# Optimization experiments

Measured on AMD Instinct MI355X. Metric: run time of the kernel, lower is better.

## Reference

```python
import jax, jax.numpy as jnp
import numpy as np

B, S, D = 4, 1024, 1024
DH = D // 8  # q/k projection dim


def setup_inputs() -> dict:
    key = jax.random.key(0)
    ks = jax.random.split(key, 16)
    std = 0.02
    inp = {
        "drums": jax.random.normal(ks[0], (B, S, D), jnp.float32),
        "vocals": jax.random.normal(ks[1], (B, S, D), jnp.float32),
        "bass": jax.random.normal(ks[2], (B, S, D), jnp.float32),
        "other": jax.random.normal(ks[3], (B, S, D), jnp.float32),
        # Linear weights stored [in, out] (transposed vs torch's [out, in])
        "DqW": jax.random.normal(ks[4], (D, DH), jnp.float32) * std,
        "Dqb": jax.random.normal(ks[5], (DH,), jnp.float32) * std,
        "DkW": jax.random.normal(ks[6], (D, DH), jnp.float32) * std,
        "Dkb": jax.random.normal(ks[7], (DH,), jnp.float32) * std,
        "DvW": jax.random.normal(ks[8], (D, D), jnp.float32) * std,
        "Dvb": jax.random.normal(ks[9], (D,), jnp.float32) * std,
        "VqW": jax.random.normal(ks[10], (D, DH), jnp.float32) * std,
        "Vqb": jax.random.normal(ks[11], (DH,), jnp.float32) * std,
        "VkW": jax.random.normal(ks[12], (D, DH), jnp.float32) * std,
        "Vkb": jax.random.normal(ks[13], (DH,), jnp.float32) * std,
        "VvW": jax.random.normal(ks[14], (D, D), jnp.float32) * std,
        "Vvb": jax.random.normal(ks[15], (D,), jnp.float32) * std,
    }
    return inp


def reference(drums, vocals, bass, other,
              DqW, Dqb, DkW, Dkb, DvW, Dvb,
              VqW, Vqb, VkW, Vkb, VvW, Vvb):
    d_model = drums.shape[-1]
    lin = lambda x, W, b: jnp.einsum("bsd,de->bse", x, W) + b
    # drums uses D_* projections; vocals/bass/other all use V_* (faithful to source)
    q = jnp.concatenate([lin(drums, DqW, Dqb), lin(vocals, VqW, Vqb),
                         lin(bass, VqW, Vqb), lin(other, VqW, Vqb)], axis=-2)
    k = jnp.concatenate([lin(drums, DkW, Dkb), lin(vocals, VkW, Vkb),
                         lin(bass, VkW, Vkb), lin(other, VkW, Vkb)], axis=-2)
    v = jnp.concatenate([lin(drums, DvW, Dvb), lin(vocals, VvW, Vvb),
                         lin(bass, VvW, Vvb), lin(other, VvW, Vvb)], axis=-2)
    # scores: [B, 4S, 4S]; dropout is identity at inference
    scores = jnp.einsum("bqe,bke->bqk", q, k) / jnp.sqrt(jnp.asarray(d_model, q.dtype))
    attn = jax.nn.softmax(scores, axis=-1)
    out = jnp.einsum("bqk,bkd->bqd", attn, v)  # [B, 4S, D]
    return out.mean(axis=-2)  # [B, D]
```

## Files before the change

### kernel.cpp

```cpp
#include <hip/hip_runtime.h>
#include <hip/hip_bf16.h>

typedef __bf16 bf16x8 __attribute__((ext_vector_type(8)));
typedef float  f32x4  __attribute__((ext_vector_type(4)));

#define MFMA(a, b, c) __builtin_amdgcn_mfma_f32_16x16x32_bf16((a), (b), (c), 0, 0, 0)

static constexpr float SC_L2E = 0.03125f * 1.44269504088896341f;
static constexpr float INV_NQ = 1.0f / 4096.0f;

__device__ inline bf16x8 ld_cvt_bf8(const float* __restrict__ p) {
    f32x4 x0 = *(const f32x4*)p;
    f32x4 x1 = *(const f32x4*)(p + 4);
    bf16x8 r;
    r[0] = (__bf16)x0[0]; r[1] = (__bf16)x0[1]; r[2] = (__bf16)x0[2]; r[3] = (__bf16)x0[3];
    r[4] = (__bf16)x1[0]; r[5] = (__bf16)x1[1]; r[6] = (__bf16)x1[2]; r[7] = (__bf16)x1[3];
    return r;
}

__global__ __launch_bounds__(256) void kT(const float* __restrict__ Dq, const float* __restrict__ Vq,
                                          const float* __restrict__ Dk, const float* __restrict__ Vk,
                                          __bf16* __restrict__ Wt) {
    __shared__ float tile[64][65];
    int bx = blockIdx.x;
    int m = bx >> 5, rt = (bx >> 1) & 15, ct = bx & 1;
    const float* W = (m == 0) ? Dq : (m == 1) ? Vq : (m == 2) ? Dk : Vk;
    int t = threadIdx.x;
    int tr = t >> 6, tc = t & 63;
#pragma unroll
    for (int i = 0; i < 16; i++) {
        int rl = tr + i * 4;
        tile[rl][tc] = W[(size_t)(rt * 64 + rl) * 128 + ct * 64 + tc];
    }
    __syncthreads();
#pragma unroll
    for (int i = 0; i < 16; i++) {
        int cl = tr + i * 4;
        Wt[(size_t)m * 131072 + (size_t)(ct * 64 + cl) * 1024 + rt * 64 + tc] = (__bf16)tile[tc][cl];
    }
}

__global__ __launch_bounds__(256) void kProj(
    const float* __restrict__ drums, const float* __restrict__ vocals,
    const float* __restrict__ bass,  const float* __restrict__ other,
    const float* __restrict__ Dqb, const float* __restrict__ Vqb,
    const float* __restrict__ Dkb, const float* __restrict__ Vkb,
    const __bf16* __restrict__ Wt, __bf16* __restrict__ Qb, __bf16* __restrict__ Kb) {
    int grow0 = blockIdx.x * 16;
    int b    = grow0 >> 12;
    int r4   = grow0 & 4095;
    int stem = r4 >> 10;
    int rin  = r4 & 1023;

    const float* X = (stem == 0) ? drums : (stem == 1) ? vocals : (stem == 2) ? bass : other;
    const __bf16* WQ = Wt + (size_t)((stem == 0) ? 0 : 1) * 131072;
    const __bf16* WK = Wt + (size_t)((stem == 0) ? 2 : 3) * 131072;
    const float* bQ = (stem == 0) ? Dqb : Vqb;
    const float* bK = (stem == 0) ? Dkb : Vkb;

    int lane = threadIdx.x & 63, wid = threadIdx.x >> 6;
    int l16 = lane & 15, g = lane >> 4;

    f32x4 aQ[2], aK[2];
#pragma unroll
    for (int j = 0; j < 2; j++) { aQ[j] = (f32x4){0.f,0.f,0.f,0.f}; aK[j] = (f32x4){0.f,0.f,0.f,0.f}; }

    const float*  xr  = X  + ((size_t)b * 1024 + rin + l16) * 1024;
    const __bf16* wq0 = WQ + (size_t)(wid * 32 + l16) * 1024;
    const __bf16* wq1 = wq0 + 16 * 1024;
    const __bf16* wk0 = WK + (size_t)(wid * 32 + l16) * 1024;
    const __bf16* wk1 = wk0 + 16 * 1024;

    for (int k0 = 0; k0 < 1024; k0 += 32) {
        int ko = k0 + g * 8;
        bf16x8 a = ld_cvt_bf8(xr + ko);
        aQ[0] = MFMA(a, *(const bf16x8*)(wq0 + ko), aQ[0]);
        aQ[1] = MFMA(a, *(const bf16x8*)(wq1 + ko), aQ[1]);
        aK[0] = MFMA(a, *(const bf16x8*)(wk0 + ko), aK[0]);
        aK[1] = MFMA(a, *(const bf16x8*)(wk1 + ko), aK[1]);
    }
    size_t obase = (size_t)b * 4096 + (size_t)stem * 1024 + rin;
#pragma unroll
    for (int cf = 0; cf < 2; cf++) {
        int col = (wid * 2 + cf) * 16 + l16;
        float bvq = bQ[col], bvk = bK[col];
#pragma unroll
        for (int r = 0; r < 4; r++) {
            int row = g * 4 + r;
            Qb[(obase + row) * 128 + col] = (__bf16)(aQ[cf][r] + bvq);
            Kb[(obase + row) * 128 + col] = (__bf16)(aK[cf][r] + bvk);
        }
    }
}

__global__ __launch_bounds__(256) void kRowSum(const __bf16* __restrict__ Qb,
                                               const __bf16* __restrict__ Kb,
                                               float* __restrict__ lsum) {
    __shared__ uint4 ktile[1024];
    int bx = blockIdx.x;
    int cc = bx & 7, tile = (bx >> 3) & 31, b = bx >> 8;
    int lane = threadIdx.x & 63, wid = threadIdx.x >> 6;
    int l16 = lane & 15, g = lane >> 4;
    int R  = tile * 128 + wid * 32;
    int C0 = cc * 512;
    const __bf16* Qr = Qb + (size_t)b * 4096 * 128;
    const __bf16* Kr = Kb + (size_t)b * 4096 * 128;

    bf16x8 a[2][4];
#pragma unroll
    for (int rf = 0; rf < 2; rf++)
#pragma unroll
        for (int kf = 0; kf < 4; kf++)
            a[rf][kf] = *(const bf16x8*)(Qr + (size_t)(R + rf * 16 + l16) * 128 + kf * 32 + g * 8);

    int sr = threadIdx.x >> 2, sseg = threadIdx.x & 3;
    char* kbc = (char*)ktile;
    int swm = (sr & 7) << 4;

    uint4 st[4];
    {
        const char* src = (const char*)(Kr + (size_t)(C0 + sr) * 128) + sseg * 64;
#pragma unroll
        for (int j = 0; j < 4; j++) st[j] = *(const uint4*)(src + j * 16);
    }

    float rs[2][4] = {};
    for (int s = 0; s < 8; ++s) {
        __syncthreads();
#pragma unroll
        for (int j = 0; j < 4; j++)
            *(uint4*)(kbc + sr * 256 + ((sseg * 64 + j * 16) ^ swm)) = st[j];
        __syncthreads();
        if (s < 7) {
            const char* src = (const char*)(Kr + (size_t)(C0 + (s + 1) * 64 + sr) * 128) + sseg * 64;
#pragma unroll
            for (int j = 0; j < 4; j++) st[j] = *(const uint4*)(src + j * 16);
        }
#pragma unroll
        for (int ctl = 0; ctl < 4; ++ctl) {
            int r2 = ctl * 16 + l16;
            int rm = (r2 & 7) << 4;
            f32x4 acc0 = (f32x4){0.f,0.f,0.f,0.f};
            f32x4 acc1 = (f32x4){0.f,0.f,0.f,0.f};
#pragma unroll
            for (int kf = 0; kf < 4; kf++) {
                bf16x8 bv = *(const bf16x8*)(kbc + r2 * 256 + ((kf * 64 + g * 16) ^ rm));
                acc0 = MFMA(a[0][kf], bv, acc0);
                acc1 = MFMA(a[1][kf], bv, acc1);
            }
#pragma unroll
            for (int r = 0; r < 4; r++) {
                rs[0][r] += exp2f(acc0[r] * SC_L2E);
                rs[1][r] += exp2f(acc1[r] * SC_L2E);
            }
        }
    }
#pragma unroll
    for (int rf = 0; rf < 2; rf++)
#pragma unroll
        for (int r = 0; r < 4; r++) {
            float v = rs[rf][r];
#pragma unroll
            for (int m = 1; m < 16; m <<= 1) v += __shfl_xor(v, m);
            if (l16 == 0) atomicAdd(&lsum[(size_t)b * 4096 + R + rf * 16 + g * 4 + r], v);
        }
}

__global__ __launch_bounds__(256) void kInv(const float* __restrict__ lsum, float* __restrict__ linv) {
    int i = (blockIdx.x * 256 + threadIdx.x) * 4;
    f32x4 v = *(const f32x4*)(lsum + i);
    f32x4 r = (f32x4){1.f / v[0], 1.f / v[1], 1.f / v[2], 1.f / v[3]};
    *(f32x4*)(linv + i) = r;
}

__global__ __launch_bounds__(256) void kColSum(const __bf16* __restrict__ Qb,
                                               const __bf16* __restrict__ Kb,
                                               const float* __restrict__ linv,
                                               float* __restrict__ wsum) {
    __shared__ uint4 qtile[1024];
    __shared__ float li[512];
    int bx = blockIdx.x;
    int rc = bx & 7, tile = (bx >> 3) & 31, b = bx >> 8;
    int lane = threadIdx.x & 63, wid = threadIdx.x >> 6;
    int l16 = lane & 15, g = lane >> 4;
    int C  = tile * 128 + wid * 32;
    int R0 = rc * 512;
    const __bf16* Qr = Qb + (size_t)b * 4096 * 128;
    const __bf16* Kr = Kb + (size_t)b * 4096 * 128;

    if (threadIdx.x < 128)
        *(f32x4*)(li + threadIdx.x * 4) = *(const f32x4*)(linv + (size_t)b * 4096 + R0 + threadIdx.x * 4);

    bf16x8 kb[2][4];
#pragma unroll
    for (int cf = 0; cf < 2; cf++)
#pragma unroll
        for (int kf = 0; kf < 4; kf++)
            kb[cf][kf] = *(const bf16x8*)(Kr + (size_t)(C + cf * 16 + l16) * 128 + kf * 32 + g * 8);

    int sr = threadIdx.x >> 2, sseg = threadIdx.x & 3;
    char* qbc = (char*)qtile;
    int swm = (sr & 7) << 4;

    uint4 st[4];
    {
        const char* src = (const char*)(Qr + (size_t)(R0 + sr) * 128) + sseg * 64;
#pragma unroll
        for (int j = 0; j < 4; j++) st[j] = *(const uint4*)(src + j * 16);
    }

    float cs[2] = {0.f, 0.f};
    for (int s = 0; s < 8; ++s) {
        __syncthreads();
#pragma unroll
        for (int j = 0; j < 4; j++)
            *(uint4*)(qbc + sr * 256 + ((sseg * 64 + j * 16) ^ swm)) = st[j];
        __syncthreads();
        if (s < 7) {
            const char* src = (const char*)(Qr + (size_t)(R0 + (s + 1) * 64 + sr) * 128) + sseg * 64;
#pragma unroll
            for (int j = 0; j < 4; j++) st[j] = *(const uint4*)(src + j * 16);
        }
#pragma unroll
        for (int ctl = 0; ctl < 4; ++ctl) {
            int r2 = ctl * 16 + l16;
            int rm = (r2 & 7) << 4;
            f32x4 acc0 = (f32x4){0.f,0.f,0.f,0.f};
            f32x4 acc1 = (f32x4){0.f,0.f,0.f,0.f};
#pragma unroll
            for (int kf = 0; kf < 4; kf++) {
                bf16x8 av = *(const bf16x8*)(qbc + r2 * 256 + ((kf * 64 + g * 16) ^ rm));
                acc0 = MFMA(av, kb[0][kf], acc0);
                acc1 = MFMA(av, kb[1][kf], acc1);
            }
            int ib = s * 64 + ctl * 16 + g * 4;
#pragma unroll
            for (int r = 0; r < 4; r++) {
                float lv = li[ib + r];
                cs[0] += exp2f(acc0[r] * SC_L2E) * lv;
                cs[1] += exp2f(acc1[r] * SC_L2E) * lv;
            }
        }
    }
#pragma unroll
    for (int cf = 0; cf < 2; cf++) {
        float v = cs[cf];
        v += __shfl_xor(v, 16);
        v += __shfl_xor(v, 32);
        if (lane < 16) atomicAdd(&wsum[(size_t)b * 4096 + C + cf * 16 + lane], v);
    }
}

__global__ __launch_bounds__(256) void kY(
    const float* __restrict__ drums, const float* __restrict__ vocals,
    const float* __restrict__ bass,  const float* __restrict__ other,
    const float* __restrict__ wsum, float* __restrict__ y, float* __restrict__ alpha) {
    __shared__ float ws[16];
    int bx = blockIdx.x;
    int b = bx >> 8, stem = (bx >> 6) & 3, kc = bx & 63;
    const float* X = (stem == 0) ? drums : (stem == 1) ? vocals : (stem == 2) ? bass : other;
    int t = threadIdx.x;
    float wv = 0.f;
    if (t < 16) { wv = wsum[(size_t)b * 4096 + stem * 1024 + kc * 16 + t] * INV_NQ; ws[t] = wv; }
    __syncthreads();

    f32x4 acc = (f32x4){0.f, 0.f, 0.f, 0.f};
    const float* xp = X + ((size_t)b * 1024 + kc * 16) * 1024 + t * 4;
#pragma unroll 4
    for (int i = 0; i < 16; i++) {
        f32x4 xv = *(const f32x4*)(xp + (size_t)i * 1024);
        float wvi = ws[i];
        acc[0] += wvi * xv[0]; acc[1] += wvi * xv[1]; acc[2] += wvi * xv[2]; acc[3] += wvi * xv[3];
    }
    int seg = (stem == 0) ? 0 : 1;
    float* yp = y + ((size_t)b * 2 + seg) * 1024 + t * 4;
    atomicAdd(yp + 0, acc[0]); atomicAdd(yp + 1, acc[1]);
    atomicAdd(yp + 2, acc[2]); atomicAdd(yp + 3, acc[3]);

    if (t < 16) {
        float s = wv;
        s += __shfl_xor(s, 1); s += __shfl_xor(s, 2);
        s += __shfl_xor(s, 4); s += __shfl_xor(s, 8);
        if (t == 0) atomicAdd(alpha + b * 2 + seg, s);
    }
}

__global__ __launch_bounds__(256) void kFinal(
    const float* __restrict__ DvW, const float* __restrict__ Dvb,
    const float* __restrict__ VvW, const float* __restrict__ Vvb,
    const float* __restrict__ y, const float* __restrict__ alpha,
    float* __restrict__ out) {
    __shared__ float yD[32], yV[32];
    int bx = blockIdx.x;
    int b = bx >> 7, dstripe = (bx >> 5) & 3, kc = bx & 31;
    int t = threadIdx.x;
    if (t < 32) {
        yD[t] = y[((size_t)b * 2 + 0) * 1024 + kc * 32 + t];
        yV[t] = y[((size_t)b * 2 + 1) * 1024 + kc * 32 + t];
    }
    __syncthreads();

    int d = dstripe * 256 + t;
    const float* pD = DvW + (size_t)(kc * 32) * 1024 + d;
    const float* pV = VvW + (size_t)(kc * 32) * 1024 + d;
    float acc = 0.f;
#pragma unroll 4
    for (int k = 0; k < 32; k++)
        acc += yD[k] * pD[(size_t)k * 1024] + yV[k] * pV[(size_t)k * 1024];
    if (kc == 0) acc += alpha[b * 2] * Dvb[d] + alpha[b * 2 + 1] * Vvb[d];
    atomicAdd(out + (size_t)b * 1024 + d, acc);
}

extern "C" void kernel_launch(void* const* d_in, const int* in_sizes, int n_in,
                              void* d_out, int out_size, void* d_ws, size_t ws_size,
                              hipStream_t stream) {
    const float* drums  = (const float*)d_in[0];
    const float* vocals = (const float*)d_in[1];
    const float* bass   = (const float*)d_in[2];
    const float* other  = (const float*)d_in[3];
    const float* DqW = (const float*)d_in[4];
    const float* Dqb = (const float*)d_in[5];
    const float* DkW = (const float*)d_in[6];
    const float* Dkb = (const float*)d_in[7];
    const float* DvW = (const float*)d_in[8];
    const float* Dvb = (const float*)d_in[9];
    const float* VqW = (const float*)d_in[10];
    const float* Vqb = (const float*)d_in[11];
    const float* VkW = (const float*)d_in[12];
    const float* Vkb = (const float*)d_in[13];
    const float* VvW = (const float*)d_in[14];
    const float* Vvb = (const float*)d_in[15];
    float* out = (float*)d_out;

    char* ws = (char*)d_ws;
    __bf16* Qb   = (__bf16*)(ws);
    __bf16* Kb   = (__bf16*)(ws + (4u << 20));
    __bf16* Wt   = (__bf16*)(ws + (8u << 20));
    float*  lsum = (float*)(ws + (9u << 20));
    float*  wsum = (float*)(ws + (9u << 20) + (64u << 10));
    float*  y    = (float*)(ws + (9u << 20) + (128u << 10));
    float*  alph = (float*)(ws + (9u << 20) + (160u << 10));
    float*  linv = (float*)(ws + (9u << 20) + (192u << 10));

    hipMemsetAsync(lsum, 0, (160u << 10) + 32, stream);
    hipMemsetAsync(out, 0, (size_t)out_size * sizeof(float), stream);

    kT<<<128, 256, 0, stream>>>(DqW, VqW, DkW, VkW, Wt);
    kProj<<<1024, 256, 0, stream>>>(drums, vocals, bass, other, Dqb, Vqb, Dkb, Vkb, Wt, Qb, Kb);
    kRowSum<<<1024, 256, 0, stream>>>(Qb, Kb, lsum);
    kInv<<<16, 256, 0, stream>>>(lsum, linv);
    kColSum<<<1024, 256, 0, stream>>>(Qb, Kb, linv, wsum);
    kY<<<1024, 256, 0, stream>>>(drums, vocals, bass, other, wsum, y, alph);
    kFinal<<<512, 256, 0, stream>>>(DvW, Dvb, VvW, Vvb, y, alph, out);
}
```

Before: 355.5 us.

## Split-K Q/K projection with LDS-staged swizzled X tiles and atomic accumulation

```diff
diff --git a/kernel.cpp b/kernel.cpp
--- a/kernel.cpp
+++ b/kernel.cpp
@@ -18,6 +18,13 @@
     return r;
 }
 
+__device__ inline bf16x8 cvt2_bf8(f32x4 a, f32x4 b) {
+    bf16x8 r;
+    r[0] = (__bf16)a[0]; r[1] = (__bf16)a[1]; r[2] = (__bf16)a[2]; r[3] = (__bf16)a[3];
+    r[4] = (__bf16)b[0]; r[5] = (__bf16)b[1]; r[6] = (__bf16)b[2]; r[7] = (__bf16)b[3];
+    return r;
+}
+
 __global__ __launch_bounds__(256) void kT(const float* __restrict__ Dq, const float* __restrict__ Vq,
                                           const float* __restrict__ Dk, const float* __restrict__ Vk,
                                           __bf16* __restrict__ Wt) {
@@ -40,57 +47,107 @@
     }
 }
 
-__global__ __launch_bounds__(256) void kProj(
+__global__ __launch_bounds__(256) void kProjP(
     const float* __restrict__ drums, const float* __restrict__ vocals,
     const float* __restrict__ bass,  const float* __restrict__ other,
-    const float* __restrict__ Dqb, const float* __restrict__ Vqb,
-    const float* __restrict__ Dkb, const float* __restrict__ Vkb,
-    const __bf16* __restrict__ Wt, __bf16* __restrict__ Qb, __bf16* __restrict__ Kb) {
-    int grow0 = blockIdx.x * 16;
-    int b    = grow0 >> 12;
-    int r4   = grow0 & 4095;
-    int stem = r4 >> 10;
-    int rin  = r4 & 1023;
+    const __bf16* __restrict__ Wt, float* __restrict__ Qf, float* __restrict__ Kf) {
+    __shared__ char xt[8192];
+    int bx = blockIdx.x;
+    int kc = bx & 3, rt = (bx >> 2) & 15, bs = bx >> 6;
+    int b = bs >> 2, stem = bs & 3;
+    int rin = rt * 64;
+    int k0b = kc * 256;
 
     const float* X = (stem == 0) ? drums : (stem == 1) ? vocals : (stem == 2) ? bass : other;
     const __bf16* WQ = Wt + (size_t)((stem == 0) ? 0 : 1) * 131072;
     const __bf16* WK = Wt + (size_t)((stem == 0) ? 2 : 3) * 131072;
-    const float* bQ = (stem == 0) ? Dqb : Vqb;
-    const float* bK = (stem == 0) ? Dkb : Vkb;
-
-    int lane = threadIdx.x & 63, wid = threadIdx.x >> 6;
+
+    int t = threadIdx.x;
+    int lane = t & 63, wid = t >> 6;
     int l16 = lane & 15, g = lane >> 4;
 
-    f32x4 aQ[2], aK[2];
-#pragma unroll
-    for (int j = 0; j < 2; j++) { aQ[j] = (f32x4){0.f,0.f,0.f,0.f}; aK[j] = (f32x4){0.f,0.f,0.f,0.f}; }
-
-    const float*  xr  = X  + ((size_t)b * 1024 + rin + l16) * 1024;
-    const __bf16* wq0 = WQ + (size_t)(wid * 32 + l16) * 1024;
-    const __bf16* wq1 = wq0 + 16 * 1024;
-    const __bf16* wk0 = WK + (size_t)(wid * 32 + l16) * 1024;
-    const __bf16* wk1 = wk0 + 16 * 1024;
-
-    for (int k0 = 0; k0 < 1024; k0 += 32) {
-        int ko = k0 + g * 8;
-        bf16x8 a = ld_cvt_bf8(xr + ko);
-        aQ[0] = MFMA(a, *(const bf16x8*)(wq0 + ko), aQ[0]);
-        aQ[1] = MFMA(a, *(const bf16x8*)(wq1 + ko), aQ[1]);
-        aK[0] = MFMA(a, *(const bf16x8*)(wk0 + ko), aK[0]);
-        aK[1] = MFMA(a, *(const bf16x8*)(wk1 + ko), aK[1]);
-    }
-    size_t obase = (size_t)b * 4096 + (size_t)stem * 1024 + rin;
-#pragma unroll
-    for (int cf = 0; cf < 2; cf++) {
-        int col = (wid * 2 + cf) * 16 + l16;
-        float bvq = bQ[col], bvk = bK[col];
-#pragma unroll
-        for (int r = 0; r < 4; r++) {
-            int row = g * 4 + r;
-            Qb[(obase + row) * 128 + col] = (__bf16)(aQ[cf][r] + bvq);
-            Kb[(obase + row) * 128 + col] = (__bf16)(aK[cf][r] + bvk);
-        }
-    }
+    const __bf16* Wm = (wid < 2) ? WQ : WK;
+    int colbase = (wid & 1) * 64;
+    float* Pf = (wid < 2) ? Qf : Kf;
+
+    int srow = t >> 2, sseg = t & 3;
+    const float* xsrc = X + ((size_t)b * 1024 + rin + srow) * 1024 + k0b + sseg * 16;
+    int swz = (srow & 7) << 4;
+    char* wrp = xt + srow * 128;
+
+    f32x4 st[4];
+#define LOADST(s) { const float* p_ = xsrc + (s) * 64; \
+    st[0] = *(const f32x4*)p_; st[1] = *(const f32x4*)(p_ + 4); \
+    st[2] = *(const f32x4*)(p_ + 8); st[3] = *(const f32x4*)(p_ + 12); }
+    LOADST(0);
+
+    f32x4 acc[4][4];
+#pragma unroll
+    for (int i = 0; i < 4; i++)
+#pragma unroll
+        for (int j = 0; j < 4; j++) acc[i][j] = (f32x4){0.f, 0.f, 0.f, 0.f};
+
+    for (int s = 0; s < 4; ++s) {
+        if (s) __syncthreads();
+        bf16x8 c0 = cvt2_bf8(st[0], st[1]);
+        bf16x8 c1 = cvt2_bf8(st[2], st[3]);
+        *(uint4*)(wrp + ((sseg * 32) ^ swz))      = *(uint4*)&c0;
+        *(uint4*)(wrp + ((sseg * 32 + 16) ^ swz)) = *(uint4*)&c1;
+        __syncthreads();
+        if (s < 3) LOADST(s + 1);
+#pragma unroll
+        for (int kk = 0; kk < 64; kk += 32) {
+            bf16x8 bfr[4];
+#pragma unroll
+            for (int cf = 0; cf < 4; cf++)
+                bfr[cf] = *(const bf16x8*)(Wm + (size_t)(colbase + cf * 16 + l16) * 1024
+                                           + k0b + s * 64 + kk + g * 8);
+#pragma unroll
+            for (int rf = 0; rf < 4; rf++) {
+                int row = rf * 16 + l16;
+                bf16x8 av = *(const bf16x8*)(xt + row * 128
+                                             + (((kk + g * 8) * 2) ^ ((row & 7) << 4)));
+#pragma unroll
+                for (int cf = 0; cf < 4; cf++)
+                    acc[rf][cf] = MFMA(av, bfr[cf], acc[rf][cf]);
+            }
+        }
+    }
+#undef LOADST
+
+    size_t grow = (size_t)b * 4096 + (size_t)stem * 1024 + rin;
+#pragma unroll
+    for (int rf = 0; rf < 4; rf++)
+#pragma unroll
+        for (int cf = 0; cf < 4; cf++) {
+            int col = colbase + cf * 16 + l16;
+#pragma unroll
+            for (int i = 0; i < 4; i++)
+                atomicAdd(&Pf[(grow + rf * 16 + g * 4 + i) * 128 + col], acc[rf][cf][i]);
+        }
+}
+
+__global__ __launch_bounds__(256) void kBias(
+    const float* __restrict__ Qf, const float* __restrict__ Kf,
+    const float* __restrict__ Dqb, const float* __restrict__ Vqb,
+    const float* __restrict__ Dkb, const float* __restrict__ Vkb,
+    __bf16* __restrict__ Qb, __bf16* __restrict__ Kb) {
+    int gid = blockIdx.x * 256 + threadIdx.x;
+    int qk  = gid >> 18;
+    int rem = gid & 262143;
+    int row = rem >> 4, ch = rem & 15;
+    int stem = (row >> 10) & 3;
+    const float* Pf   = qk ? Kf : Qf;
+    const float* bias = qk ? ((stem == 0) ? Dkb : Vkb) : ((stem == 0) ? Dqb : Vqb);
+    __bf16* Out = qk ? Kb : Qb;
+    int col = ch * 8;
+    f32x4 v0 = *(const f32x4*)(Pf + (size_t)row * 128 + col);
+    f32x4 v1 = *(const f32x4*)(Pf + (size_t)row * 128 + col + 4);
+    f32x4 b0 = *(const f32x4*)(bias + col);
+    f32x4 b1 = *(const f32x4*)(bias + col + 4);
+    bf16x8 r = cvt2_bf8((f32x4){v0[0]+b0[0], v0[1]+b0[1], v0[2]+b0[2], v0[3]+b0[3]},
+                        (f32x4){v1[0]+b1[0], v1[1]+b1[1], v1[2]+b1[2], v1[3]+b1[3]});
+    *(bf16x8*)(Out + (size_t)row * 128 + col) = r;
 }
 
 __global__ __launch_bounds__(256) void kRowSum(const __bf16* __restrict__ Qb,
@@ -341,12 +398,16 @@
     float*  y    = (float*)(ws + (9u << 20) + (128u << 10));
     float*  alph = (float*)(ws + (9u << 20) + (160u << 10));
     float*  linv = (float*)(ws + (9u << 20) + (192u << 10));
+    float*  Qf   = (float*)(ws + (10u << 20));
+    float*  Kf   = (float*)(ws + (18u << 20));
 
     hipMemsetAsync(lsum, 0, (160u << 10) + 32, stream);
+    hipMemsetAsync(Qf, 0, (16u << 20), stream);
     hipMemsetAsync(out, 0, (size_t)out_size * sizeof(float), stream);
 
     kT<<<128, 256, 0, stream>>>(DqW, VqW, DkW, VkW, Wt);
-    kProj<<<1024, 256, 0, stream>>>(drums, vocals, bass, other, Dqb, Vqb, Dkb, Vkb, Wt, Qb, Kb);
+    kProjP<<<1024, 256, 0, stream>>>(drums, vocals, bass, other, Wt, Qf, Kf);
+    kBias<<<2048, 256, 0, stream>>>(Qf, Kf, Dqb, Vqb, Dkb, Vkb, Qb, Kb);
     kRowSum<<<1024, 256, 0, stream>>>(Qb, Kb, lsum);
     kInv<<<16, 256, 0, stream>>>(lsum, linv);
     kColSum<<<1024, 256, 0, stream>>>(Qb, Kb, linv, wsum);
```

Measured after the change: 345.9 us. 1.03x faster.

## Stage X tiles through LDS in projection kernel and split score kernels finer

Applied to the files above, without the earlier changes.

```diff
diff --git a/kernel.cpp b/kernel.cpp
--- a/kernel.cpp
+++ b/kernel.cpp
@@ -2,21 +2,13 @@
 #include <hip/hip_bf16.h>
 
 typedef __bf16 bf16x8 __attribute__((ext_vector_type(8)));
+typedef __bf16 bf16x4 __attribute__((ext_vector_type(4)));
 typedef float  f32x4  __attribute__((ext_vector_type(4)));
 
 #define MFMA(a, b, c) __builtin_amdgcn_mfma_f32_16x16x32_bf16((a), (b), (c), 0, 0, 0)
 
 static constexpr float SC_L2E = 0.03125f * 1.44269504088896341f;
 static constexpr float INV_NQ = 1.0f / 4096.0f;
-
-__device__ inline bf16x8 ld_cvt_bf8(const float* __restrict__ p) {
-    f32x4 x0 = *(const f32x4*)p;
-    f32x4 x1 = *(const f32x4*)(p + 4);
-    bf16x8 r;
-    r[0] = (__bf16)x0[0]; r[1] = (__bf16)x0[1]; r[2] = (__bf16)x0[2]; r[3] = (__bf16)x0[3];
-    r[4] = (__bf16)x1[0]; r[5] = (__bf16)x1[1]; r[6] = (__bf16)x1[2]; r[7] = (__bf16)x1[3];
-    return r;
-}
 
 __global__ __launch_bounds__(256) void kT(const float* __restrict__ Dq, const float* __restrict__ Vq,
                                           const float* __restrict__ Dk, const float* __restrict__ Vk,
@@ -40,56 +32,80 @@
     }
 }
 
-__global__ __launch_bounds__(256) void kProj(
+__global__ __launch_bounds__(256, 4) void kProj2(
     const float* __restrict__ drums, const float* __restrict__ vocals,
     const float* __restrict__ bass,  const float* __restrict__ other,
     const float* __restrict__ Dqb, const float* __restrict__ Vqb,
     const float* __restrict__ Dkb, const float* __restrict__ Vkb,
     const __bf16* __restrict__ Wt, __bf16* __restrict__ Qb, __bf16* __restrict__ Kb) {
-    int grow0 = blockIdx.x * 16;
-    int b    = grow0 >> 12;
-    int r4   = grow0 & 4095;
-    int stem = r4 >> 10;
-    int rin  = r4 & 1023;
+    __shared__ uint4 xt4[128];
+    char* xt = (char*)xt4;
+    int bx = blockIdx.x;
+    int rt = bx & 63, bs = bx >> 6;
+    int b = bs >> 2, stem = bs & 3;
+    int rin = rt * 16;
 
     const float* X = (stem == 0) ? drums : (stem == 1) ? vocals : (stem == 2) ? bass : other;
     const __bf16* WQ = Wt + (size_t)((stem == 0) ? 0 : 1) * 131072;
     const __bf16* WK = Wt + (size_t)((stem == 0) ? 2 : 3) * 131072;
-    const float* bQ = (stem == 0) ? Dqb : Vqb;
-    const float* bK = (stem == 0) ? Dkb : Vkb;
-
-    int lane = threadIdx.x & 63, wid = threadIdx.x >> 6;
+
+    int t = threadIdx.x, lane = t & 63, wid = t >> 6;
     int l16 = lane & 15, g = lane >> 4;
 
-    f32x4 aQ[2], aK[2];
-#pragma unroll
-    for (int j = 0; j < 2; j++) { aQ[j] = (f32x4){0.f,0.f,0.f,0.f}; aK[j] = (f32x4){0.f,0.f,0.f,0.f}; }
-
-    const float*  xr  = X  + ((size_t)b * 1024 + rin + l16) * 1024;
-    const __bf16* wq0 = WQ + (size_t)(wid * 32 + l16) * 1024;
-    const __bf16* wq1 = wq0 + 16 * 1024;
-    const __bf16* wk0 = WK + (size_t)(wid * 32 + l16) * 1024;
-    const __bf16* wk1 = wk0 + 16 * 1024;
-
-    for (int k0 = 0; k0 < 1024; k0 += 32) {
-        int ko = k0 + g * 8;
-        bf16x8 a = ld_cvt_bf8(xr + ko);
-        aQ[0] = MFMA(a, *(const bf16x8*)(wq0 + ko), aQ[0]);
-        aQ[1] = MFMA(a, *(const bf16x8*)(wq1 + ko), aQ[1]);
-        aK[0] = MFMA(a, *(const bf16x8*)(wk0 + ko), aK[0]);
-        aK[1] = MFMA(a, *(const bf16x8*)(wk1 + ko), aK[1]);
-    }
-    size_t obase = (size_t)b * 4096 + (size_t)stem * 1024 + rin;
-#pragma unroll
-    for (int cf = 0; cf < 2; cf++) {
-        int col = (wid * 2 + cf) * 16 + l16;
-        float bvq = bQ[col], bvk = bK[col];
-#pragma unroll
-        for (int r = 0; r < 4; r++) {
-            int row = g * 4 + r;
-            Qb[(obase + row) * 128 + col] = (__bf16)(aQ[cf][r] + bvq);
-            Kb[(obase + row) * 128 + col] = (__bf16)(aK[cf][r] + bvk);
-        }
+    const __bf16* Wm   = (wid < 2) ? WQ : WK;
+    const float*  bias = (wid < 2) ? ((stem == 0) ? Dqb : Vqb) : ((stem == 0) ? Dkb : Vkb);
+    __bf16*       Out  = (wid < 2) ? Qb : Kb;
+    int colbase = (wid & 1) * 64;
+
+    int srow = t >> 4, sc4 = t & 15;
+    const float* xsrc = X + ((size_t)b * 1024 + rin + srow) * 1024 + sc4 * 4;
+    int swz = (srow & 7) << 4;
+    char* wrp = xt + srow * 128;
+    int wb = sc4 * 8;
+
+    const __bf16* wp = Wm + (size_t)(colbase + l16) * 1024;
+
+    f32x4 stg = *(const f32x4*)xsrc;
+    bf16x8 bcur[4], bnxt[4];
+#pragma unroll
+    for (int cf = 0; cf < 4; cf++) bcur[cf] = *(const bf16x8*)(wp + cf * 16384 + g * 8);
+
+    f32x4 acc[4];
+#pragma unroll
+    for (int cf = 0; cf < 4; cf++) acc[cf] = (f32x4){0.f, 0.f, 0.f, 0.f};
+
+    for (int s = 0; s < 16; ++s) {
+        if (s) __syncthreads();
+        bf16x4 c;
+        c[0] = (__bf16)stg[0]; c[1] = (__bf16)stg[1];
+        c[2] = (__bf16)stg[2]; c[3] = (__bf16)stg[3];
+        *(bf16x4*)(wrp + (wb ^ swz)) = c;
+        __syncthreads();
+        if (s < 15) stg = *(const f32x4*)(xsrc + (s + 1) * 64);
+#pragma unroll
+        for (int kk = 0; kk < 2; ++kk) {
+            if (kk == 0 || s < 15) {
+                int knk = (kk == 0) ? s * 64 + 32 : (s + 1) * 64;
+#pragma unroll
+                for (int cf = 0; cf < 4; cf++)
+                    bnxt[cf] = *(const bf16x8*)(wp + cf * 16384 + knk + g * 8);
+            }
+            bf16x8 av = *(const bf16x8*)(xt + l16 * 128 + ((kk * 64 + g * 16) ^ ((l16 & 7) << 4)));
+#pragma unroll
+            for (int cf = 0; cf < 4; cf++) acc[cf] = MFMA(av, bcur[cf], acc[cf]);
+#pragma unroll
+            for (int cf = 0; cf < 4; cf++) bcur[cf] = bnxt[cf];
+        }
+    }
+
+    size_t grow = (size_t)b * 4096 + (size_t)stem * 1024 + rin;
+#pragma unroll
+    for (int cf = 0; cf < 4; cf++) {
+        int col = colbase + cf * 16 + l16;
+        float bv = bias[col];
+#pragma unroll
+        for (int i = 0; i < 4; i++)
+            Out[(grow + g * 4 + i) * 128 + col] = (__bf16)(acc[cf][i] + bv);
     }
 }
 
@@ -98,11 +114,11 @@
                                                float* __restrict__ lsum) {
     __shared__ uint4 ktile[1024];
     int bx = blockIdx.x;
-    int cc = bx & 7, tile = (bx >> 3) & 31, b = bx >> 8;
+    int cc = bx & 15, tile = (bx >> 4) & 31, b = bx >> 9;
     int lane = threadIdx.x & 63, wid = threadIdx.x >> 6;
     int l16 = lane & 15, g = lane >> 4;
     int R  = tile * 128 + wid * 32;
-    int C0 = cc * 512;
+    int C0 = cc * 256;
     const __bf16* Qr = Qb + (size_t)b * 4096 * 128;
     const __bf16* Kr = Kb + (size_t)b * 4096 * 128;
 
@@ -125,13 +141,13 @@
     }
 
     float rs[2][4] = {};
-    for (int s = 0; s < 8; ++s) {
+    for (int s = 0; s < 4; ++s) {
         __syncthreads();
 #pragma unroll
         for (int j = 0; j < 4; j++)
             *(uint4*)(kbc + sr * 256 + ((sseg * 64 + j * 16) ^ swm)) = st[j];
         __syncthreads();
-        if (s < 7) {
+        if (s < 3) {
             const char* src = (const char*)(Kr + (size_t)(C0 + (s + 1) * 64 + sr) * 128) + sseg * 64;
 #pragma unroll
             for (int j = 0; j < 4; j++) st[j] = *(const uint4*)(src + j * 16);
@@ -178,17 +194,17 @@
                                                const float* __restrict__ linv,
                                                float* __restrict__ wsum) {
     __shared__ uint4 qtile[1024];
-    __shared__ float li[512];
-    int bx = blockIdx.x;
-    int rc = bx & 7, tile = (bx >> 3) & 31, b = bx >> 8;
+    __shared__ float li[256];
+    int bx = blockIdx.x;
+    int rc = bx & 15, tile = (bx >> 4) & 31, b = bx >> 9;
     int lane = threadIdx.x & 63, wid = threadIdx.x >> 6;
     int l16 = lane & 15, g = lane >> 4;
     int C  = tile * 128 + wid * 32;
-    int R0 = rc * 512;
+    int R0 = rc * 256;
     const __bf16* Qr = Qb + (size_t)b * 4096 * 128;
     const __bf16* Kr = Kb + (size_t)b * 4096 * 128;
 
-    if (threadIdx.x < 128)
+    if (threadIdx.x < 64)
         *(f32x4*)(li + threadIdx.x * 4) = *(const f32x4*)(linv + (size_t)b * 4096 + R0 + threadIdx.x * 4);
 
     bf16x8 kb[2][4];
@@ -210,13 +226,13 @@
     }
 
     float cs[2] = {0.f, 0.f};
-    for (int s = 0; s < 8; ++s) {
+    for (int s = 0; s < 4; ++s) {
         __syncthreads();
 #pragma unroll
         for (int j = 0; j < 4; j++)
             *(uint4*)(qbc + sr * 256 + ((sseg * 64 + j * 16) ^ swm)) = st[j];
         __syncthreads();
-        if (s < 7) {
+        if (s < 3) {
             const char* src = (const char*)(Qr + (size_t)(R0 + (s + 1) * 64 + sr) * 128) + sseg * 64;
 #pragma unroll
             for (int j = 0; j < 4; j++) st[j] = *(const uint4*)(src + j * 16);
@@ -346,10 +362,10 @@
     hipMemsetAsync(out, 0, (size_t)out_size * sizeof(float), stream);
 
     kT<<<128, 256, 0, stream>>>(DqW, VqW, DkW, VkW, Wt);
-    kProj<<<1024, 256, 0, stream>>>(drums, vocals, bass, other, Dqb, Vqb, Dkb, Vkb, Wt, Qb, Kb);
-    kRowSum<<<1024, 256, 0, stream>>>(Qb, Kb, lsum);
+    kProj2<<<1024, 256, 0, stream>>>(drums, vocals, bass, other, Dqb, Vqb, Dkb, Vkb, Wt, Qb, Kb);
+    kRowSum<<<2048, 256, 0, stream>>>(Qb, Kb, lsum);
     kInv<<<16, 256, 0, stream>>>(lsum, linv);
-    kColSum<<<1024, 256, 0, stream>>>(Qb, Kb, linv, wsum);
+    kColSum<<<2048, 256, 0, stream>>>(Qb, Kb, linv, wsum);
     kY<<<1024, 256, 0, stream>>>(drums, vocals, bass, other, wsum, y, alph);
     kFinal<<<512, 256, 0, stream>>>(DvW, Dvb, VvW, Vvb, y, alph, out);
 }
```

New measurement: 341.6 us. -3.9%, faster.
